# Performance work log

Hardware: AMD Instinct MI355X
Metric: run time of the kernel (lower is better)

## Reference

```python
import jax, jax.numpy as jnp
import numpy as np

N = 100000
E = 1600000
C_IN = 128
C_HID = 128


def setup_inputs() -> dict:
    key = jax.random.key(0)
    ks = jax.random.split(key, 6)
    x = jax.random.normal(ks[0], (N, C_IN), dtype=jnp.float32)
    edge_index = jax.random.randint(ks[1], (2, E), 0, N, dtype=jnp.int64)
    # GCNConv params: linear weight + bias per layer (glorot-ish scale)
    W1 = jax.random.normal(ks[2], (C_IN, C_HID), dtype=jnp.float32) / np.sqrt(C_IN)
    b1 = jnp.zeros((C_HID,), dtype=jnp.float32)
    W2 = jax.random.normal(ks[3], (C_HID, C_HID), dtype=jnp.float32) / np.sqrt(C_HID)
    b2 = jnp.zeros((C_HID,), dtype=jnp.float32)
    return {"x": x, "edge_index": edge_index, "W1": W1, "b1": b1, "W2": W2, "b2": b2}


def _gcn_conv(x, W, b, src, dst, n_nodes):
    # PyG GCNConv: h = D^{-1/2} (A + I) D^{-1/2} (x W) + b
    h = x @ W  # [N, C_out]
    # add self-loops
    loop = jnp.arange(n_nodes, dtype=src.dtype)
    s = jnp.concatenate([src, loop])
    d = jnp.concatenate([dst, loop])
    ones = jnp.ones(s.shape[0], dtype=h.dtype)
    deg = jax.ops.segment_sum(ones, d, num_segments=n_nodes)  # in-degree incl self-loop
    dinv = jnp.where(deg > 0, jax.lax.rsqrt(deg), 0.0)
    norm = dinv[s] * dinv[d]  # [E+N]
    msg = h[s] * norm[:, None]  # gather + scale
    out = jax.ops.segment_sum(msg, d, num_segments=n_nodes)  # scatter-add
    return out + b


def reference(x, edge_index, W1, b1, W2, b2):
    src, dst = edge_index[0], edge_index[1]
    h = jax.nn.relu(_gcn_conv(x, W1, b1, src, dst, N))
    h = jax.nn.relu(_gcn_conv(h, W2, b2, src, dst, N))
    return h
```

## Files before the change

### kernel.cpp

```cpp
#include <hip/hip_runtime.h>
#include <hip/hip_bf16.h>

#define GCN_N 100000
#define GB1 1563
#define NBUCK 782
#define BCAP 4096
#define KPWG 391

typedef unsigned short u16;
typedef unsigned int u32;
typedef float f32x4 __attribute__((ext_vector_type(4)));
typedef short bf16x8 __attribute__((ext_vector_type(8)));

union v16 { uint4 u; bf16x8 h; };

__device__ inline u16 f2bf(float f) {
    u32 u = __float_as_uint(f);
    return (u16)((u + 0x7fffu + ((u >> 16) & 1u)) >> 16);
}
__device__ inline u32 pack2(float a, float b) {
    return (u32)f2bf(a) | ((u32)f2bf(b) << 16);
}
__device__ inline float bf_lo(u32 u) { return __uint_as_float(u << 16); }
__device__ inline float bf_hi(u32 u) { return __uint_as_float(u & 0xffff0000u); }
__device__ inline u32 scale2(u32 p, float d) {
    return pack2(bf_lo(p) * d, bf_hi(p) * d);
}

__device__ inline void addu8(float* a, float4 v) {
    u32 u;
    u = __float_as_uint(v.x); a[0] += bf_lo(u); a[1] += bf_hi(u);
    u = __float_as_uint(v.y); a[2] += bf_lo(u); a[3] += bf_hi(u);
    u = __float_as_uint(v.z); a[4] += bf_lo(u); a[5] += bf_hi(u);
    u = __float_as_uint(v.w); a[6] += bf_lo(u); a[7] += bf_hi(u);
}
__device__ inline void setu8(float* a, float4 v) {
    u32 u;
    u = __float_as_uint(v.x); a[0] = bf_lo(u); a[1] = bf_hi(u);
    u = __float_as_uint(v.y); a[2] = bf_lo(u); a[3] = bf_hi(u);
    u = __float_as_uint(v.z); a[4] = bf_lo(u); a[5] = bf_hi(u);
    u = __float_as_uint(v.w); a[6] = bf_lo(u); a[7] = bf_hi(u);
}

__device__ inline void mfma16(f32x4& d, uint4 a, uint4 b) {
    v16 av, bv; av.u = a; bv.u = b;
    d = __builtin_amdgcn_mfma_f32_16x16x32_bf16(av.h, bv.h, d, 0, 0, 0);
}

__global__ __launch_bounds__(256) void k_init(int* __restrict__ gcursor,
                                              const float* __restrict__ W1,
                                              const float* __restrict__ W2,
                                              u16* __restrict__ Wt1,
                                              u16* __restrict__ Wt2) {
    if (blockIdx.x == 0) {
        for (int i = threadIdx.x; i < NBUCK; i += 256) gcursor[i] = 0;
        return;
    }
    const float* W = (blockIdx.x == 1) ? W1 : W2;
    u16* Wt = (blockIdx.x == 1) ? Wt1 : Wt2;
    for (int i = threadIdx.x; i < 16384; i += 256) {
        int k = i >> 7, nn = i & 127;
        Wt[nn * 128 + k] = f2bf(W[i]);
    }
}

template<int SCALE>
__device__ __attribute__((always_inline))
inline void gemm_core(const uint4* Xs, const u16* __restrict__ Wt,
                      const float* __restrict__ dinv, u16* __restrict__ H,
                      long long row0, int n) {
    const int t = threadIdx.x;
    const int wid = t >> 6;
    const int l = t & 63, lm = l & 15, lh = l >> 4;
    uint4 a[4];
    const int lrow = wid * 16 + lm;
    #pragma unroll
    for (int kk = 0; kk < 4; ++kk) {
        int byte = (lrow * 256 + kk * 64 + lh * 16) ^ ((lm & 7) << 4);
        a[kk] = Xs[byte >> 4];
    }
    const uint4* wb = (const uint4*)Wt;
    f32x4 acc[8];
    #pragma unroll
    for (int j = 0; j < 8; ++j) acc[j] = (f32x4){0.f, 0.f, 0.f, 0.f};
    #pragma unroll
    for (int j = 0; j < 8; ++j) {
        #pragma unroll
        for (int kk = 0; kk < 4; ++kk) {
            uint4 b = wb[(j * 16 + lm) * 16 + kk * 4 + lh];
            mfma16(acc[j], a[kk], b);
        }
    }
    long long gr0 = row0 + wid * 16 + lh * 4;
    float dv[4];
    #pragma unroll
    for (int r = 0; r < 4; ++r)
        dv[r] = SCALE ? ((gr0 + r < n) ? dinv[gr0 + r] : 0.f) : 1.f;
    #pragma unroll
    for (int j = 0; j < 8; ++j) {
        #pragma unroll
        for (int r = 0; r < 4; ++r) {
            long long grow = gr0 + r;
            if (grow < n)
                H[grow * 128 + j * 16 + lm] =
                    f2bf(SCALE ? acc[j][r] * dv[r] : acc[j][r]);
        }
    }
}

__global__ __launch_bounds__(256) void k_part_gemm1(
        const int* __restrict__ src, const int* __restrict__ dst,
        int* __restrict__ gcursor, u32* __restrict__ part,
        const float* __restrict__ X, const u16* __restrict__ Wt,
        u16* __restrict__ H, int E, int n) {
    __shared__ uint4 Xs[1024];
    if (blockIdx.x < KPWG) {
        int* lhist = (int*)Xs;
        int* lbase = lhist + NBUCK;
        int* lcur  = lbase + NBUCK;
        const int t = threadIdx.x;
        for (int i = t; i < NBUCK; i += 256) { lhist[i] = 0; lcur[i] = 0; }
        __syncthreads();
        const long long e0 = (long long)blockIdx.x * 4096;
        #pragma unroll
        for (int i = 0; i < 16; ++i) {
            long long e = e0 + i * 256 + t;
            if (e < E) atomicAdd(&lhist[dst[e] >> 7], 1);
        }
        __syncthreads();
        for (int i = t; i < NBUCK; i += 256) {
            int c = lhist[i];
            lbase[i] = c ? atomicAdd(&gcursor[i], c) : 0;
        }
        __syncthreads();
        #pragma unroll
        for (int i = 0; i < 16; ++i) {
            long long e = e0 + i * 256 + t;
            if (e < E) {
                int d = dst[e];
                int b = d >> 7;
                int ofs = lbase[b] + atomicAdd(&lcur[b], 1);
                if (ofs < BCAP)
                    part[(long long)b * BCAP + ofs] =
                        (u32)src[e] | ((u32)(d & 127) << 17);
            }
        }
        return;
    }
    const long long row0 = (long long)(blockIdx.x - KPWG) * 64;
    const int t = threadIdx.x;
    uint2* Xs2 = (uint2*)Xs;
    #pragma unroll
    for (int i = 0; i < 8; ++i) {
        int idx = i * 1024 + t * 4;
        int row = idx >> 7, k = idx & 127;
        long long grow = row0 + row; if (grow >= n) grow = n - 1;
        float4 v = *(const float4*)(X + grow * 128 + k);
        int byte = (row * 256 + k * 2) ^ ((row & 7) << 4);
        uint2 p; p.x = pack2(v.x, v.y); p.y = pack2(v.z, v.w);
        Xs2[byte >> 3] = p;
    }
    __syncthreads();
    gemm_core<0>(Xs, Wt, nullptr, H, row0, n);
}

__global__ __launch_bounds__(256) void k_csr(const int* __restrict__ gcursor,
                                             const u32* __restrict__ part,
                                             int* __restrict__ rowstart,
                                             float* __restrict__ dinv,
                                             int* __restrict__ csr,
                                             u16* __restrict__ h1, int n) {
    __shared__ int lcount[128];
    __shared__ int lpfx[128];
    __shared__ int lcur[128];
    __shared__ float ldinv[128];
    __shared__ int wpart[4];
    __shared__ int sbase;
    const int t = threadIdx.x;
    const int lane = t & 63, wid = t >> 6;
    const int b = blockIdx.x;
    int ps = 0;
    for (int j = t; j < b; j += 256) ps += min(gcursor[j], BCAP);
    #pragma unroll
    for (int off = 32; off > 0; off >>= 1) ps += __shfl_down(ps, off, 64);
    if (lane == 0) wpart[wid] = ps;
    if (t < 128) { lcount[t] = 0; lcur[t] = 0; }
    __syncthreads();
    if (t == 0) sbase = wpart[0] + wpart[1] + wpart[2] + wpart[3];
    __syncthreads();
    const int base = sbase;
    const int cnt = min(gcursor[b], BCAP);
    const u32* bp = part + (long long)b * BCAP;
    for (int i = t; i < cnt; i += 256) atomicAdd(&lcount[bp[i] >> 17], 1);
    __syncthreads();
    if (t == 0) {
        int run = 0;
        #pragma unroll
        for (int j = 0; j < 128; ++j) { lpfx[j] = run; run += lcount[j]; }
    }
    __syncthreads();
    int node = b * 128 + t;
    if (t < 128) {
        float dv = rsqrtf((float)(lcount[t] + 1));
        ldinv[t] = dv;
        if (node < n) {
            rowstart[node] = base + lpfx[t];
            dinv[node] = dv;
        }
    }
    if (b == NBUCK - 1 && t == 0) rowstart[n] = base + cnt;
    __syncthreads();
    for (int i = t; i < cnt; i += 256) {
        u32 v = bp[i];
        int loc = v >> 17;
        int p = base + lpfx[loc] + atomicAdd(&lcur[loc], 1);
        csr[p] = (int)(v & 0x1FFFFu);
    }
    uint4* h4 = (uint4*)h1;
    const long long rbase = (long long)b * 128;
    for (int i = t; i < 2048; i += 256) {
        int loc = i >> 4;
        long long nd = rbase + loc;
        if (nd < n) {
            float d = ldinv[loc];
            long long gi = nd * 16 + (i & 15);
            uint4 v = h4[gi];
            v.x = scale2(v.x, d); v.y = scale2(v.y, d);
            v.z = scale2(v.z, d); v.w = scale2(v.w, d);
            h4[gi] = v;
        }
    }
}

__global__ __launch_bounds__(256) void k_gemm2(
        const u16* __restrict__ X, const u16* __restrict__ Wt,
        const float* __restrict__ dinv, u16* __restrict__ H, int n) {
    __shared__ uint4 Xs[1024];
    const long long row0 = (long long)blockIdx.x * 64;
    const int t = threadIdx.x;
    #pragma unroll
    for (int i = 0; i < 4; ++i) {
        int idx = i * 2048 + t * 8;
        int row = idx >> 7, k = idx & 127;
        long long grow = row0 + row; if (grow >= n) grow = n - 1;
        uint4 v = *(const uint4*)(X + grow * 128 + k);
        int byte = (row * 256 + k * 2) ^ ((row & 7) << 4);
        Xs[byte >> 4] = v;
    }
    __syncthreads();
    gemm_core<1>(Xs, Wt, dinv, H, row0, n);
}

template<int OUT_BF16>
__global__ __launch_bounds__(256) void k_agg(const u16* __restrict__ h,
                                             const int* __restrict__ rowstart,
                                             const int* __restrict__ csr_src,
                                             const float* __restrict__ dinv,
                                             const float* __restrict__ bias,
                                             void* __restrict__ outp, int n) {
    const int q    = threadIdx.x >> 4;
    const int sub  = threadIdx.x & 15;
    const int node = blockIdx.x * 16 + q;
    if (node >= n) return;
    const float di = dinv[node];
    int e = rowstart[node];
    const int end = rowstart[node + 1];
    const float4* __restrict__ hv = (const float4*)h;
    float a[8], b[8];
    setu8(a, hv[(size_t)node * 16 + sub]);
    #pragma unroll
    for (int j = 0; j < 8; ++j) b[j] = 0.f;
    for (; e + 8 <= end; e += 8) {
        int s0 = csr_src[e + 0], s1 = csr_src[e + 1];
        int s2 = csr_src[e + 2], s3 = csr_src[e + 3];
        int s4 = csr_src[e + 4], s5 = csr_src[e + 5];
        int s6 = csr_src[e + 6], s7 = csr_src[e + 7];
        float4 v0 = hv[(size_t)s0 * 16 + sub];
        float4 v1 = hv[(size_t)s1 * 16 + sub];
        float4 v2 = hv[(size_t)s2 * 16 + sub];
        float4 v3 = hv[(size_t)s3 * 16 + sub];
        float4 v4 = hv[(size_t)s4 * 16 + sub];
        float4 v5 = hv[(size_t)s5 * 16 + sub];
        float4 v6 = hv[(size_t)s6 * 16 + sub];
        float4 v7 = hv[(size_t)s7 * 16 + sub];
        addu8(a, v0); addu8(b, v1); addu8(a, v2); addu8(b, v3);
        addu8(a, v4); addu8(b, v5); addu8(a, v6); addu8(b, v7);
    }
    for (; e + 4 <= end; e += 4) {
        int s0 = csr_src[e + 0], s1 = csr_src[e + 1];
        int s2 = csr_src[e + 2], s3 = csr_src[e + 3];
        float4 v0 = hv[(size_t)s0 * 16 + sub];
        float4 v1 = hv[(size_t)s1 * 16 + sub];
        float4 v2 = hv[(size_t)s2 * 16 + sub];
        float4 v3 = hv[(size_t)s3 * 16 + sub];
        addu8(a, v0); addu8(b, v1); addu8(a, v2); addu8(b, v3);
    }
    for (; e < end; ++e) {
        float4 v = hv[(size_t)csr_src[e] * 16 + sub];
        addu8(a, v);
    }
    const float4 bv0 = ((const float4*)bias)[sub * 2];
    const float4 bv1 = ((const float4*)bias)[sub * 2 + 1];
    float o[8];
    o[0] = fmaxf(fmaf(a[0] + b[0], di, bv0.x), 0.f);
    o[1] = fmaxf(fmaf(a[1] + b[1], di, bv0.y), 0.f);
    o[2] = fmaxf(fmaf(a[2] + b[2], di, bv0.z), 0.f);
    o[3] = fmaxf(fmaf(a[3] + b[3], di, bv0.w), 0.f);
    o[4] = fmaxf(fmaf(a[4] + b[4], di, bv1.x), 0.f);
    o[5] = fmaxf(fmaf(a[5] + b[5], di, bv1.y), 0.f);
    o[6] = fmaxf(fmaf(a[6] + b[6], di, bv1.z), 0.f);
    o[7] = fmaxf(fmaf(a[7] + b[7], di, bv1.w), 0.f);
    if (OUT_BF16) {
        float4 pv;
        pv.x = __uint_as_float(pack2(o[0], o[1]));
        pv.y = __uint_as_float(pack2(o[2], o[3]));
        pv.z = __uint_as_float(pack2(o[4], o[5]));
        pv.w = __uint_as_float(pack2(o[6], o[7]));
        ((float4*)outp)[(size_t)node * 16 + sub] = pv;
    } else {
        float* out = (float*)outp + (size_t)node * 128 + sub * 8;
        float4 w0 = {o[0], o[1], o[2], o[3]};
        float4 w1 = {o[4], o[5], o[6], o[7]};
        *(float4*)(out + 0) = w0;
        *(float4*)(out + 4) = w1;
    }
}


extern "C" void kernel_launch(void* const* d_in, const int* in_sizes, int n_in,
                              void* d_out, int out_size, void* d_ws, size_t ws_size,
                              hipStream_t stream) {
    const float* x   = (const float*)d_in[0];
    const int* edges = (const int*)d_in[1];
    const float* W1  = (const float*)d_in[2];
    const float* b1  = (const float*)d_in[3];
    const float* W2  = (const float*)d_in[4];
    const float* b2  = (const float*)d_in[5];
    const int E = in_sizes[1] / 2;
    const int N = GCN_N;
    const int* srcp = edges;
    const int* dstp = edges + E;

    char* ws = (char*)d_ws;
    int*   gcursor  = (int*)(ws + 0);
    int*   rowstart = (int*)(ws + 4096);
    float* dinvp    = (float*)(ws + 413696);
    u16*   wt1      = (u16*)(ws + 819200);
    u16*   wt2      = (u16*)(ws + 851968);
    u32*   part     = (u32*)(ws + 1048576);
    int*   csr      = (int*)(ws + 14680064);
    u16*   h1       = (u16*)(ws + 23068672);
    u16*   h2       = (u16*)(ws + 50331648);

    k_init<<<3, 256, 0, stream>>>(gcursor, W1, W2, wt1, wt2);
    k_part_gemm1<<<KPWG + GB1, 256, 0, stream>>>(srcp, dstp, gcursor, part,
                                                 x, wt1, h1, E, N);
    k_csr<<<NBUCK, 256, 0, stream>>>(gcursor, part, rowstart, dinvp, csr, h1, N);
    k_agg<1><<<(N + 15) / 16, 256, 0, stream>>>(h1, rowstart, csr, dinvp, b1, h2, N);
    k_gemm2<<<GB1, 256, 0, stream>>>(h2, wt2, dinvp, h1, N);
    k_agg<0><<<(N + 15) / 16, 256, 0, stream>>>(h1, rowstart, csr, dinvp, b2, d_out, N);
}
```

Measured before the change: 259.3 us.

## Fuse layer-1 aggregation into GEMM2 and widen partition buckets to 256 nodes

The first-layer aggregation now runs inside the GEMM2 kernel. Each block aggregates its 64 rows directly into swizzled shared memory, so the bf16 intermediate no longer makes a round trip through global memory and one launch is removed. Partition buckets now cover 256 destination nodes each (391 buckets, capacity 8192). Fewer, larger partition workgroups each handle 16384 edges, and the CSR kernel processes 256 nodes per block. Risks: less parallelism in the partition and CSR phases, the serial prefix scan over 256 entries, and lower occupancy for the fused aggregation since each GEMM block aggregates 64 rows before it computes.

```diff
diff --git a/kernel.cpp b/kernel.cpp
--- a/kernel.cpp
+++ b/kernel.cpp
@@ -3,9 +3,9 @@
 
 #define GCN_N 100000
 #define GB1 1563
-#define NBUCK 782
-#define BCAP 4096
-#define KPWG 391
+#define NBUCK 391
+#define BCAP 8192
+#define KPWG 98
 
 typedef unsigned short u16;
 typedef unsigned int u32;
@@ -121,11 +121,10 @@
         const int t = threadIdx.x;
         for (int i = t; i < NBUCK; i += 256) { lhist[i] = 0; lcur[i] = 0; }
         __syncthreads();
-        const long long e0 = (long long)blockIdx.x * 4096;
-        #pragma unroll
-        for (int i = 0; i < 16; ++i) {
+        const long long e0 = (long long)blockIdx.x * 16384;
+        for (int i = 0; i < 64; ++i) {
             long long e = e0 + i * 256 + t;
-            if (e < E) atomicAdd(&lhist[dst[e] >> 7], 1);
+            if (e < E) atomicAdd(&lhist[dst[e] >> 8], 1);
         }
         __syncthreads();
         for (int i = t; i < NBUCK; i += 256) {
@@ -133,16 +132,15 @@
             lbase[i] = c ? atomicAdd(&gcursor[i], c) : 0;
         }
         __syncthreads();
-        #pragma unroll
-        for (int i = 0; i < 16; ++i) {
+        for (int i = 0; i < 64; ++i) {
             long long e = e0 + i * 256 + t;
             if (e < E) {
                 int d = dst[e];
-                int b = d >> 7;
+                int b = d >> 8;
                 int ofs = lbase[b] + atomicAdd(&lcur[b], 1);
                 if (ofs < BCAP)
                     part[(long long)b * BCAP + ofs] =
-                        (u32)src[e] | ((u32)(d & 127) << 17);
+                        (u32)src[e] | ((u32)(d & 255) << 17);
             }
         }
         return;
@@ -170,21 +168,21 @@
                                              float* __restrict__ dinv,
                                              int* __restrict__ csr,
                                              u16* __restrict__ h1, int n) {
-    __shared__ int lcount[128];
-    __shared__ int lpfx[128];
-    __shared__ int lcur[128];
-    __shared__ float ldinv[128];
+    __shared__ int lcount[256];
+    __shared__ int lpfx[256];
+    __shared__ int lcur[256];
+    __shared__ float ldinv[256];
     __shared__ int wpart[4];
     __shared__ int sbase;
     const int t = threadIdx.x;
     const int lane = t & 63, wid = t >> 6;
     const int b = blockIdx.x;
-    int ps = 0;
-    for (int j = t; j < b; j += 256) ps += min(gcursor[j], BCAP);
+    int ps = ((t < b) ? min(gcursor[t], BCAP) : 0) +
+             ((t + 256 < b) ? min(gcursor[t + 256], BCAP) : 0);
     #pragma unroll
     for (int off = 32; off > 0; off >>= 1) ps += __shfl_down(ps, off, 64);
     if (lane == 0) wpart[wid] = ps;
-    if (t < 128) { lcount[t] = 0; lcur[t] = 0; }
+    lcount[t] = 0; lcur[t] = 0;
     __syncthreads();
     if (t == 0) sbase = wpart[0] + wpart[1] + wpart[2] + wpart[3];
     __syncthreads();
@@ -195,12 +193,12 @@
     __syncthreads();
     if (t == 0) {
         int run = 0;
-        #pragma unroll
-        for (int j = 0; j < 128; ++j) { lpfx[j] = run; run += lcount[j]; }
-    }
-    __syncthreads();
-    int node = b * 128 + t;
-    if (t < 128) {
+        #pragma unroll 8
+        for (int j = 0; j < 256; ++j) { lpfx[j] = run; run += lcount[j]; }
+    }
+    __syncthreads();
+    int node = b * 256 + t;
+    {
         float dv = rsqrtf((float)(lcount[t] + 1));
         ldinv[t] = dv;
         if (node < n) {
@@ -217,8 +215,8 @@
         csr[p] = (int)(v & 0x1FFFFu);
     }
     uint4* h4 = (uint4*)h1;
-    const long long rbase = (long long)b * 128;
-    for (int i = t; i < 2048; i += 256) {
+    const long long rbase = (long long)b * 256;
+    for (int i = t; i < 4096; i += 256) {
         int loc = i >> 4;
         long long nd = rbase + loc;
         if (nd < n) {
@@ -232,32 +230,76 @@
     }
 }
 
-__global__ __launch_bounds__(256) void k_gemm2(
-        const u16* __restrict__ X, const u16* __restrict__ Wt,
-        const float* __restrict__ dinv, u16* __restrict__ H, int n) {
+__global__ __launch_bounds__(256) void k_agg_gemm2(
+        const u16* __restrict__ h, const int* __restrict__ rowstart,
+        const int* __restrict__ csr_src, const float* __restrict__ dinv,
+        const float* __restrict__ bias, const u16* __restrict__ Wt,
+        u16* __restrict__ H3, int n) {
     __shared__ uint4 Xs[1024];
     const long long row0 = (long long)blockIdx.x * 64;
-    const int t = threadIdx.x;
-    #pragma unroll
-    for (int i = 0; i < 4; ++i) {
-        int idx = i * 2048 + t * 8;
-        int row = idx >> 7, k = idx & 127;
-        long long grow = row0 + row; if (grow >= n) grow = n - 1;
-        uint4 v = *(const uint4*)(X + grow * 128 + k);
-        int byte = (row * 256 + k * 2) ^ ((row & 7) << 4);
-        Xs[byte >> 4] = v;
-    }
-    __syncthreads();
-    gemm_core<1>(Xs, Wt, dinv, H, row0, n);
-}
-
-template<int OUT_BF16>
-__global__ __launch_bounds__(256) void k_agg(const u16* __restrict__ h,
-                                             const int* __restrict__ rowstart,
-                                             const int* __restrict__ csr_src,
-                                             const float* __restrict__ dinv,
-                                             const float* __restrict__ bias,
-                                             void* __restrict__ outp, int n) {
+    const int q   = threadIdx.x >> 4;
+    const int sub = threadIdx.x & 15;
+    const float4* __restrict__ hv = (const float4*)h;
+    const float4 bv0 = ((const float4*)bias)[sub * 2];
+    const float4 bv1 = ((const float4*)bias)[sub * 2 + 1];
+    #pragma unroll 1
+    for (int rr = 0; rr < 4; ++rr) {
+        const int row = rr * 16 + q;
+        const long long node = row0 + row;
+        uint4 pv = {0, 0, 0, 0};
+        if (node < n) {
+            const float di = dinv[node];
+            int e = rowstart[node];
+            const int end = rowstart[node + 1];
+            float a[8], b[8];
+            setu8(a, hv[(size_t)node * 16 + sub]);
+            #pragma unroll
+            for (int j = 0; j < 8; ++j) b[j] = 0.f;
+            for (; e + 8 <= end; e += 8) {
+                int s0 = csr_src[e + 0], s1 = csr_src[e + 1];
+                int s2 = csr_src[e + 2], s3 = csr_src[e + 3];
+                int s4 = csr_src[e + 4], s5 = csr_src[e + 5];
+                int s6 = csr_src[e + 6], s7 = csr_src[e + 7];
+                float4 v0 = hv[(size_t)s0 * 16 + sub];
+                float4 v1 = hv[(size_t)s1 * 16 + sub];
+                float4 v2 = hv[(size_t)s2 * 16 + sub];
+                float4 v3 = hv[(size_t)s3 * 16 + sub];
+                float4 v4 = hv[(size_t)s4 * 16 + sub];
+                float4 v5 = hv[(size_t)s5 * 16 + sub];
+                float4 v6 = hv[(size_t)s6 * 16 + sub];
+                float4 v7 = hv[(size_t)s7 * 16 + sub];
+                addu8(a, v0); addu8(b, v1); addu8(a, v2); addu8(b, v3);
+                addu8(a, v4); addu8(b, v5); addu8(a, v6); addu8(b, v7);
+            }
+            for (; e < end; ++e) {
+                float4 v = hv[(size_t)csr_src[e] * 16 + sub];
+                addu8(a, v);
+            }
+            float o[8];
+            o[0] = fmaxf(fmaf(a[0] + b[0], di, bv0.x), 0.f);
+            o[1] = fmaxf(fmaf(a[1] + b[1], di, bv0.y), 0.f);
+            o[2] = fmaxf(fmaf(a[2] + b[2], di, bv0.z), 0.f);
+            o[3] = fmaxf(fmaf(a[3] + b[3], di, bv0.w), 0.f);
+            o[4] = fmaxf(fmaf(a[4] + b[4], di, bv1.x), 0.f);
+            o[5] = fmaxf(fmaf(a[5] + b[5], di, bv1.y), 0.f);
+            o[6] = fmaxf(fmaf(a[6] + b[6], di, bv1.z), 0.f);
+            o[7] = fmaxf(fmaf(a[7] + b[7], di, bv1.w), 0.f);
+            pv.x = pack2(o[0], o[1]); pv.y = pack2(o[2], o[3]);
+            pv.z = pack2(o[4], o[5]); pv.w = pack2(o[6], o[7]);
+        }
+        int byte = (row * 256 + sub * 16) ^ ((row & 7) << 4);
+        Xs[byte >> 4] = pv;
+    }
+    __syncthreads();
+    gemm_core<1>(Xs, Wt, dinv, H3, row0, n);
+}
+
+__global__ __launch_bounds__(256) void k_agg2(const u16* __restrict__ h,
+                                              const int* __restrict__ rowstart,
+                                              const int* __restrict__ csr_src,
+                                              const float* __restrict__ dinv,
+                                              const float* __restrict__ bias,
+                                              float* __restrict__ out, int n) {
     const int q    = threadIdx.x >> 4;
     const int sub  = threadIdx.x & 15;
     const int node = blockIdx.x * 16 + q;
@@ -310,20 +352,11 @@
     o[5] = fmaxf(fmaf(a[5] + b[5], di, bv1.y), 0.f);
     o[6] = fmaxf(fmaf(a[6] + b[6], di, bv1.z), 0.f);
     o[7] = fmaxf(fmaf(a[7] + b[7], di, bv1.w), 0.f);
-    if (OUT_BF16) {
-        float4 pv;
-        pv.x = __uint_as_float(pack2(o[0], o[1]));
-        pv.y = __uint_as_float(pack2(o[2], o[3]));
-        pv.z = __uint_as_float(pack2(o[4], o[5]));
-        pv.w = __uint_as_float(pack2(o[6], o[7]));
-        ((float4*)outp)[(size_t)node * 16 + sub] = pv;
-    } else {
-        float* out = (float*)outp + (size_t)node * 128 + sub * 8;
-        float4 w0 = {o[0], o[1], o[2], o[3]};
-        float4 w1 = {o[4], o[5], o[6], o[7]};
-        *(float4*)(out + 0) = w0;
-        *(float4*)(out + 4) = w1;
-    }
+    float* op = out + (size_t)node * 128 + sub * 8;
+    float4 w0 = {o[0], o[1], o[2], o[3]};
+    float4 w1 = {o[4], o[5], o[6], o[7]};
+    *(float4*)(op + 0) = w0;
+    *(float4*)(op + 4) = w1;
 }
 
 
@@ -350,13 +383,13 @@
     u32*   part     = (u32*)(ws + 1048576);
     int*   csr      = (int*)(ws + 14680064);
     u16*   h1       = (u16*)(ws + 23068672);
-    u16*   h2       = (u16*)(ws + 50331648);
+    u16*   h3       = (u16*)(ws + 50331648);
 
     k_init<<<3, 256, 0, stream>>>(gcursor, W1, W2, wt1, wt2);
     k_part_gemm1<<<KPWG + GB1, 256, 0, stream>>>(srcp, dstp, gcursor, part,
                                                  x, wt1, h1, E, N);
     k_csr<<<NBUCK, 256, 0, stream>>>(gcursor, part, rowstart, dinvp, csr, h1, N);
-    k_agg<1><<<(N + 15) / 16, 256, 0, stream>>>(h1, rowstart, csr, dinvp, b1, h2, N);
-    k_gemm2<<<GB1, 256, 0, stream>>>(h2, wt2, dinvp, h1, N);
-    k_agg<0><<<(N + 15) / 16, 256, 0, stream>>>(h1, rowstart, csr, dinvp, b2, d_out, N);
-}
+    k_agg_gemm2<<<GB1, 256, 0, stream>>>(h1, rowstart, csr, dinvp, b1, wt2, h3, N);
+    k_agg2<<<(N + 15) / 16, 256, 0, stream>>>(h3, rowstart, csr, dinvp, b2,
+                                              (float*)d_out, N);
+}
```

After: 306.2 us. 1.18x slower.
